# Kernel tuning notes

Hardware: AMD Instinct MI355X
Metric: run time of the kernel (lower is better)

## Reference

```python
import jax, jax.numpy as jnp
import numpy as np

N_NODES = 100000
N_EDGES = 3200000
EMBED_DIM = 64
BATCH = 16384


def setup_inputs() -> dict:
    key = jax.random.key(0)
    k1, k2, k3, k4 = jax.random.split(key, 4)
    gcn_weight = jax.random.normal(k1, (N_NODES, EMBED_DIM), dtype=jnp.float32) * 0.1
    gcn_bias = jnp.zeros((EMBED_DIM,), dtype=jnp.float32)
    linear_weight = jax.random.normal(k2, (N_NODES, 1), dtype=jnp.float32) * 0.1
    linear_bias = jnp.zeros((1,), dtype=jnp.float32)
    edge_index = jax.random.randint(k3, (2, N_EDGES), 0, N_NODES, dtype=jnp.int64)
    interaction_pairs = jax.random.randint(k4, (BATCH, 2), 0, N_NODES, dtype=jnp.int64)
    return {
        "gcn_weight": gcn_weight,
        "gcn_bias": gcn_bias,
        "linear_weight": linear_weight,
        "linear_bias": linear_bias,
        "edge_index": edge_index,
        "interaction_pairs": interaction_pairs,
    }


def _gcn_conv_identity_features(gcn_weight, gcn_bias, edge_index):
    # Features X = I, so X @ W = W. GCNConv output = D^{-1/2}(A+I)D^{-1/2} W + b.
    src, dst = edge_index[0], edge_index[1]
    ones = jnp.ones((src.shape[0],), dtype=gcn_weight.dtype)
    # degree (with self loop) computed on destination nodes, as in PyG gcn_norm
    deg = jax.ops.segment_sum(ones, dst, num_segments=N_NODES) + 1.0
    dinv = jax.lax.rsqrt(deg)  # [N]
    norm = dinv[src] * dinv[dst]  # [E]
    msg = gcn_weight[src] * norm[:, None]  # [E, D] -- dominant memory traffic
    agg = jax.ops.segment_sum(msg, dst, num_segments=N_NODES)  # [N, D]
    # self-loop term: norm_ii = 1/deg[i]
    out = agg + gcn_weight * (dinv * dinv)[:, None] + gcn_bias
    return out


def reference(gcn_weight, gcn_bias, linear_weight, linear_bias, edge_index, interaction_pairs):
    node_emb = _gcn_conv_identity_features(gcn_weight, gcn_bias, edge_index)  # [N, D]
    e = node_emb[interaction_pairs]  # [B, 2, D] gather
    # FM pairwise interaction: 0.5 * sum_d ((sum_f e)^2 - sum_f e^2)
    sum_sq = jnp.square(jnp.sum(e, axis=1))  # [B, D]
    sq_sum = jnp.sum(jnp.square(e), axis=1)  # [B, D]
    fm = 0.5 * jnp.sum(sum_sq - sq_sum, axis=1, keepdims=True)  # [B, 1]
    # FeaturesLinear: sum of per-node scalar embeddings + bias
    lin = jnp.sum(linear_weight[interaction_pairs], axis=1) + linear_bias  # [B, 1]
    return jnp.squeeze(lin + fm, axis=1)  # [B]
```

## Files before the change

### kernel.cpp

```cpp
#include <hip/hip_runtime.h>

#define N_NODES 100000
#define N_EDGES 3200000
#define BATCH 16384
#define MAX_SLOTS 32768

#define NW 12500
#define NW4 3125
#define SLICES 256
#define EPS2 12500
#define I4PS2 3125

#define NBUCK 512
#define BCAP 4096
#define BCAP_SH 12
#define EBCAP 4608
#define EBCAP4 1152

#define HIST_THREADS 1024
#define HGSIZE (SLICES * HIST_THREADS)

#define OFF_SLOT      0
#define OFF_DINV      400000
#define OFF_NODELIST  800000
#define OFF_GCUR      931072
#define OFF_PARTIALS  933120
#define OFF_WH        13733120
#define OFF_BINS      26533120
#define OFF_EMB       34921728

__device__ __forceinline__ unsigned bfr(float f) {
    unsigned u = __float_as_uint(f);
    return (u + 0x7FFFu + ((u >> 16) & 1u)) >> 16;
}
__device__ __forceinline__ float bfx(unsigned h) {
    return __uint_as_float(h << 16);
}

__global__ void k_flags(const int* __restrict__ pairs, unsigned* __restrict__ slot,
                        int* __restrict__ nodelist, unsigned* __restrict__ gcur) {
    int i = blockIdx.x * blockDim.x + threadIdx.x;
    if (i < NBUCK) gcur[i] = (unsigned)(i << BCAP_SH);
    if (i < 2 * BATCH) {
        int n = pairs[i];
        nodelist[i] = n;
        slot[n] = (unsigned)(i + 1);
    }
}

__device__ __forceinline__ int cert(int d, const unsigned* __restrict__ slot,
                                    const int* __restrict__ nodelist) {
    unsigned r = slot[d];
    unsigned idx = r - 1u;
    if (idx < (unsigned)MAX_SLOTS && nodelist[idx] == d) return (int)idx;
    return -1;
}

__global__ void k_hist(const int* __restrict__ src, const int* __restrict__ dst,
                       const unsigned* __restrict__ slot, const int* __restrict__ nodelist,
                       unsigned* __restrict__ partials, unsigned* __restrict__ gcur,
                       unsigned* __restrict__ bins,
                       const float4* __restrict__ w4, uint4* __restrict__ wh4) {
    __shared__ unsigned h[NW];
    __shared__ unsigned ebuf[EBCAP];
    __shared__ int lc[NBUCK];
    __shared__ int base[NBUCK];
    __shared__ int ecnt;
    int g = blockIdx.x;
    int tid = threadIdx.x;
    int lane = tid & 63;
    uint4* h4 = (uint4*)h;
    for (int i = tid; i < NW4; i += HIST_THREADS) h4[i] = make_uint4(0u, 0u, 0u, 0u);
    if (tid < NBUCK) lc[tid] = 0;
    if (tid == 0) ecnt = 0;
    __syncthreads();
    const int4* d4 = (const int4*)(dst + g * EPS2);
    const int4* s4 = (const int4*)(src + g * EPS2);
    for (int i = tid; i < I4PS2; i += HIST_THREADS) {
        int4 v = d4[i];
        int4 s = s4[i];
        atomicAdd(&h[v.x >> 3], 1u << ((v.x & 7) << 2));
        atomicAdd(&h[v.y >> 3], 1u << ((v.y & 7) << 2));
        atomicAdd(&h[v.z >> 3], 1u << ((v.z & 7) << 2));
        atomicAdd(&h[v.w >> 3], 1u << ((v.w & 7) << 2));
#define STAGE(dc, sc)                                                          \
        {                                                                      \
            int t = cert(dc, slot, nodelist);                                  \
            unsigned long long mk = __ballot(t >= 0);                          \
            int bs = 0;                                                        \
            if (lane == 0) bs = atomicAdd(&ecnt, (int)__popcll(mk));           \
            bs = __shfl(bs, 0, 64);                                            \
            if (t >= 0) {                                                      \
                int off = bs + (int)__popcll(mk & ((1ull << lane) - 1ull));    \
                if (off < EBCAP) {                                             \
                    ebuf[off] = ((unsigned)t << 17) | (unsigned)(sc);          \
                    atomicAdd(&lc[t >> 6], 1);                                 \
                }                                                              \
            }                                                                  \
        }
        STAGE(v.x, s.x)
        STAGE(v.y, s.y)
        STAGE(v.z, s.z)
        STAGE(v.w, s.w)
#undef STAGE
    }
    __syncthreads();
    uint4* outp4 = (uint4*)(partials + (unsigned)g * NW);
    for (int i = tid; i < NW4; i += HIST_THREADS) outp4[i] = h4[i];
    if (tid < NBUCK) {
        base[tid] = (int)atomicAdd(&gcur[tid], (unsigned)lc[tid]);
        lc[tid] = 0;
    }
    __syncthreads();
    int ne = ecnt;
    if (ne > EBCAP) ne = EBCAP;
    const uint4* ebuf4 = (const uint4*)ebuf;
    for (int j4 = tid; j4 * 4 < ne; j4 += HIST_THREADS) {
        uint4 e4 = ebuf4[j4];
#define FLUSH(ee, kk)                                                          \
        if (j4 * 4 + kk < ne) {                                                \
            unsigned e = (ee);                                                 \
            int b = (int)(e >> 23);                               \
            int r = atomicAdd(&lc[b], 1);                                      \
            unsigned pos = (unsigned)base[b] + (unsigned)r;                    \
            if (pos < (unsigned)((b + 1) << BCAP_SH)) bins[pos] = e;           \
        }
        FLUSH(e4.x, 0)
        FLUSH(e4.y, 1)
        FLUSH(e4.z, 2)
        FLUSH(e4.w, 3)
#undef FLUSH
    }
    for (int k = g * HIST_THREADS + tid; k < N_NODES * 8; k += HGSIZE) {
        float4 va = w4[k * 2];
        float4 vb = w4[k * 2 + 1];
        uint4 o;
        o.x = bfr(va.x) | (bfr(va.y) << 16);
        o.y = bfr(va.z) | (bfr(va.w) << 16);
        o.z = bfr(vb.x) | (bfr(vb.y) << 16);
        o.w = bfr(vb.z) | (bfr(vb.w) << 16);
        wh4[k] = o;
    }
}

__global__ void k_mid(const unsigned* __restrict__ partials, float* __restrict__ dinv) {
    __shared__ unsigned pA[256], pB[256], pC[256], pD[256];
    int blk = blockIdx.x;
    int wi = threadIdx.x & 31, sg = threadIdx.x >> 5;
    int w = blk * 32 + wi;
    unsigned A = 0, B = 0, C = 0, D = 0;
    if (w < NW) {
        const unsigned* q = partials + w;
#pragma unroll
        for (int ch = 0; ch < 2; ++ch) {
            unsigned x = 0, y = 0;
#pragma unroll
            for (int k = 0; k < 16; ++k) {
                unsigned v = q[(unsigned)(sg * 32 + ch * 16 + k) * NW];
                x += v & 0x0F0F0F0Fu;
                y += (v >> 4) & 0x0F0F0F0Fu;
            }
            A += x & 0x00FF00FFu;
            B += (x >> 8) & 0x00FF00FFu;
            C += y & 0x00FF00FFu;
            D += (y >> 8) & 0x00FF00FFu;
        }
    }
    pA[threadIdx.x] = A; pB[threadIdx.x] = B; pC[threadIdx.x] = C; pD[threadIdx.x] = D;
    __syncthreads();
    if (threadIdx.x < 32 && w < NW) {
        unsigned sA = 0, sB = 0, sC = 0, sD = 0;
#pragma unroll
        for (int k = 0; k < 8; ++k) {
            sA += pA[k * 32 + wi]; sB += pB[k * 32 + wi];
            sC += pC[k * 32 + wi]; sD += pD[k * 32 + wi];
        }
        float4 d0, d1;
        d0.x = rsqrtf((float)(sA & 0xFFFFu) + 1.0f);
        d0.y = rsqrtf((float)(sC & 0xFFFFu) + 1.0f);
        d0.z = rsqrtf((float)(sB & 0xFFFFu) + 1.0f);
        d0.w = rsqrtf((float)(sD & 0xFFFFu) + 1.0f);
        d1.x = rsqrtf((float)(sA >> 16) + 1.0f);
        d1.y = rsqrtf((float)(sC >> 16) + 1.0f);
        d1.z = rsqrtf((float)(sB >> 16) + 1.0f);
        d1.w = rsqrtf((float)(sD >> 16) + 1.0f);
        ((float4*)dinv)[w * 2] = d0;
        ((float4*)dinv)[w * 2 + 1] = d1;
    }
}

__global__ void k_gfuse(const unsigned* __restrict__ gcur, const unsigned* __restrict__ bins,
                        const int* __restrict__ nodelist, const uint4* __restrict__ wh4,
                        const float* __restrict__ dinv, const float4* __restrict__ bias4,
                        uint4* __restrict__ emb4) {
    __shared__ unsigned ebuf2[BCAP];
    __shared__ int lc[64], st[64];
    int b = blockIdx.x;
    int tid = threadIdx.x;
    int cnt = (int)(gcur[b] - (unsigned)(b << BCAP_SH));
    if (cnt > BCAP) cnt = BCAP;
    const unsigned* bp = bins + ((unsigned)b << BCAP_SH);
    if (tid < 64) lc[tid] = 0;
    __syncthreads();
    for (int j = tid; j < cnt; j += 1024) atomicAdd(&lc[(bp[j] >> 17) & 63], 1);
    __syncthreads();
    if (tid < 64) st[tid] = lc[tid];
    __syncthreads();
    for (int off = 1; off < 64; off <<= 1) {
        int v = (tid < 64 && tid >= off) ? st[tid - off] : 0;
        __syncthreads();
        if (tid < 64) st[tid] += v;
        __syncthreads();
    }
    if (tid < 64) {
        st[tid] -= lc[tid];
        lc[tid] = st[tid];
    }
    __syncthreads();
    for (int j = tid; j < cnt; j += 1024) {
        unsigned e = bp[j];
        int r = atomicAdd(&lc[(e >> 17) & 63], 1);
        ebuf2[r] = e & 0x1FFFFu;
    }
    __syncthreads();
    int wave = tid >> 6, lane = tid & 63;
    int rg = lane >> 3, dp = lane & 7;
#pragma unroll 1
    for (int q = 0; q < 4; ++q) {
        int sl = wave * 4 + q;
        int s0 = st[sl];
        int cn = lc[sl] - s0;
        double a0 = 0., a1 = 0., a2 = 0., a3 = 0., a4 = 0., a5 = 0., a6 = 0., a7 = 0.;
        int j = 0;
        for (; j + 16 <= cn; j += 16) {
            int e0 = (int)ebuf2[s0 + j + rg];
            int e1 = (int)ebuf2[s0 + j + 8 + rg];
            float dv0 = dinv[e0], dv1 = dinv[e1];
            uint4 oa = wh4[(e0 << 3) + dp];
            uint4 ob = wh4[(e1 << 3) + dp];
            a0 += (double)(bfx(oa.x) * dv0 + bfx(ob.x) * dv1);
            a1 += (double)(bfx(oa.x >> 16) * dv0 + bfx(ob.x >> 16) * dv1);
            a2 += (double)(bfx(oa.y) * dv0 + bfx(ob.y) * dv1);
            a3 += (double)(bfx(oa.y >> 16) * dv0 + bfx(ob.y >> 16) * dv1);
            a4 += (double)(bfx(oa.z) * dv0 + bfx(ob.z) * dv1);
            a5 += (double)(bfx(oa.z >> 16) * dv0 + bfx(ob.z >> 16) * dv1);
            a6 += (double)(bfx(oa.w) * dv0 + bfx(ob.w) * dv1);
            a7 += (double)(bfx(oa.w >> 16) * dv0 + bfx(ob.w >> 16) * dv1);
        }
        for (; j < cn; j += 8) {
            if (rg < cn - j) {
                int e0 = (int)ebuf2[s0 + j + rg];
                float dv0 = dinv[e0];
                uint4 oa = wh4[(e0 << 3) + dp];
                a0 += (double)(bfx(oa.x) * dv0);
                a1 += (double)(bfx(oa.x >> 16) * dv0);
                a2 += (double)(bfx(oa.y) * dv0);
                a3 += (double)(bfx(oa.y >> 16) * dv0);
                a4 += (double)(bfx(oa.z) * dv0);
                a5 += (double)(bfx(oa.z >> 16) * dv0);
                a6 += (double)(bfx(oa.w) * dv0);
                a7 += (double)(bfx(oa.w >> 16) * dv0);
            }
        }
#pragma unroll
        for (int m = 8; m <= 32; m <<= 1) {
            a0 += __shfl_xor(a0, m, 64); a1 += __shfl_xor(a1, m, 64);
            a2 += __shfl_xor(a2, m, 64); a3 += __shfl_xor(a3, m, 64);
            a4 += __shfl_xor(a4, m, 64); a5 += __shfl_xor(a5, m, 64);
            a6 += __shfl_xor(a6, m, 64); a7 += __shfl_xor(a7, m, 64);
        }
        if (rg == 0) {
            int gslot = (b << 6) + sl;
            int n = nodelist[gslot];
            float dn = dinv[n];
            uint4 u = wh4[(n << 3) + dp];
            float4 b0 = bias4[dp * 2], b1 = bias4[dp * 2 + 1];
            float r0 = ((float)a0 + bfx(u.x) * dn) * dn + b0.x;
            float r1 = ((float)a1 + bfx(u.x >> 16) * dn) * dn + b0.y;
            float r2 = ((float)a2 + bfx(u.y) * dn) * dn + b0.z;
            float r3 = ((float)a3 + bfx(u.y >> 16) * dn) * dn + b0.w;
            float r4 = ((float)a4 + bfx(u.z) * dn) * dn + b1.x;
            float r5 = ((float)a5 + bfx(u.z >> 16) * dn) * dn + b1.y;
            float r6 = ((float)a6 + bfx(u.w) * dn) * dn + b1.z;
            float r7 = ((float)a7 + bfx(u.w >> 16) * dn) * dn + b1.w;
            uint4 o;
            o.x = bfr(r0) | (bfr(r1) << 16);
            o.y = bfr(r2) | (bfr(r3) << 16);
            o.z = bfr(r4) | (bfr(r5) << 16);
            o.w = bfr(r6) | (bfr(r7) << 16);
            emb4[(gslot << 3) + dp] = o;
        }
    }
}

__global__ void k_final(const int* __restrict__ pairs, const unsigned* __restrict__ slot,
                        const uint2* __restrict__ emb2, const float* __restrict__ lw,
                        const float* __restrict__ lb, float* __restrict__ out) {
    int p = (blockIdx.x * blockDim.x + threadIdx.x) >> 4;
    int li = threadIdx.x & 15;
    if (p >= BATCH) return;
    int a = pairs[p * 2], b = pairs[p * 2 + 1];
    int sa = (int)slot[a] - 1;
    int sb = (int)slot[b] - 1;
    uint2 ua = emb2[(sa << 4) + li];
    uint2 ub = emb2[(sb << 4) + li];
    float prod = bfx(ua.x) * bfx(ub.x) + bfx(ua.x >> 16) * bfx(ub.x >> 16)
               + bfx(ua.y) * bfx(ub.y) + bfx(ua.y >> 16) * bfx(ub.y >> 16);
#pragma unroll
    for (int m = 1; m <= 8; m <<= 1) prod += __shfl_xor(prod, m, 64);
    if (li == 0) out[p] = lw[a] + lw[b] + lb[0] + prod;
}

extern "C" void kernel_launch(void* const* d_in, const int* in_sizes, int n_in,
                              void* d_out, int out_size, void* d_ws, size_t ws_size,
                              hipStream_t stream) {
    const float* gcn_weight    = (const float*)d_in[0];
    const float* gcn_bias      = (const float*)d_in[1];
    const float* linear_weight = (const float*)d_in[2];
    const float* linear_bias   = (const float*)d_in[3];
    const int*   edge_index    = (const int*)d_in[4];
    const int*   pairs         = (const int*)d_in[5];
    float* out = (float*)d_out;

    char* ws = (char*)d_ws;
    unsigned* slot      = (unsigned*)(ws + OFF_SLOT);
    float*    dinv      = (float*)   (ws + OFF_DINV);
    int*      nodelist  = (int*)     (ws + OFF_NODELIST);
    unsigned* gcur      = (unsigned*)(ws + OFF_GCUR);
    unsigned* partials  = (unsigned*)(ws + OFF_PARTIALS);
    uint4*    wh4       = (uint4*)   (ws + OFF_WH);
    unsigned* bins      = (unsigned*)(ws + OFF_BINS);
    uint4*    emb4      = (uint4*)   (ws + OFF_EMB);
    uint2*    emb2      = (uint2*)   (ws + OFF_EMB);

    const int* src_arr = edge_index;
    const int* dst_arr = edge_index + N_EDGES;

    k_flags<<<64, 512, 0, stream>>>(pairs, slot, nodelist, gcur);
    k_hist<<<SLICES, HIST_THREADS, 0, stream>>>(src_arr, dst_arr, slot, nodelist,
                                                partials, gcur, bins,
                                                (const float4*)gcn_weight, wh4);
    k_mid<<<391, 256, 0, stream>>>(partials, dinv);
    k_gfuse<<<NBUCK, 1024, 0, stream>>>(gcur, bins, nodelist, wh4,
                                        dinv, (const float4*)gcn_bias, emb4);
    k_final<<<1024, 256, 0, stream>>>(pairs, slot, emb2, linear_weight, linear_bias, out);
}
```

Measured before the change: 161.5 us.

## Double histogram slices and zero slot table to drop nodelist verification

Raises the number of histogram blocks from 256 to 512, each handling about half as many edges, and resizes the partials buffer, workspace offsets and the k_mid reduction loop to match. Adds a kernel that zeroes the slot table every call, so k_hist can test slot[d] != 0 directly instead of also checking nodelist. That removes one dependent global load per edge. In exchange it adds a kernel launch, doubles the partial-histogram traffic that k_mid has to reduce, and shrinks the per-block edge buffer, which raises the risk of dropping entries if a block overflows it.

```diff
diff --git a/kernel.cpp b/kernel.cpp
--- a/kernel.cpp
+++ b/kernel.cpp
@@ -7,15 +7,14 @@
 
 #define NW 12500
 #define NW4 3125
-#define SLICES 256
-#define EPS2 12500
-#define I4PS2 3125
+#define SLICES 512
+#define NI4 800000
+#define M4 1563
 
 #define NBUCK 512
 #define BCAP 4096
 #define BCAP_SH 12
-#define EBCAP 4608
-#define EBCAP4 1152
+#define EBCAP 2560
 
 #define HIST_THREADS 1024
 #define HGSIZE (SLICES * HIST_THREADS)
@@ -25,9 +24,9 @@
 #define OFF_NODELIST  800000
 #define OFF_GCUR      931072
 #define OFF_PARTIALS  933120
-#define OFF_WH        13733120
-#define OFF_BINS      26533120
-#define OFF_EMB       34921728
+#define OFF_WH        26533120
+#define OFF_BINS      39333120
+#define OFF_EMB       47721728
 
 __device__ __forceinline__ unsigned bfr(float f) {
     unsigned u = __float_as_uint(f);
@@ -35,6 +34,11 @@
 }
 __device__ __forceinline__ float bfx(unsigned h) {
     return __uint_as_float(h << 16);
+}
+
+__global__ void k_zero(unsigned* __restrict__ slot) {
+    int i = blockIdx.x * blockDim.x + threadIdx.x;
+    if (i < N_NODES) slot[i] = 0u;
 }
 
 __global__ void k_flags(const int* __restrict__ pairs, unsigned* __restrict__ slot,
@@ -48,16 +52,8 @@
     }
 }
 
-__device__ __forceinline__ int cert(int d, const unsigned* __restrict__ slot,
-                                    const int* __restrict__ nodelist) {
-    unsigned r = slot[d];
-    unsigned idx = r - 1u;
-    if (idx < (unsigned)MAX_SLOTS && nodelist[idx] == d) return (int)idx;
-    return -1;
-}
-
 __global__ void k_hist(const int* __restrict__ src, const int* __restrict__ dst,
-                       const unsigned* __restrict__ slot, const int* __restrict__ nodelist,
+                       const unsigned* __restrict__ slot,
                        unsigned* __restrict__ partials, unsigned* __restrict__ gcur,
                        unsigned* __restrict__ bins,
                        const float4* __restrict__ w4, uint4* __restrict__ wh4) {
@@ -74,9 +70,12 @@
     if (tid < NBUCK) lc[tid] = 0;
     if (tid == 0) ecnt = 0;
     __syncthreads();
-    const int4* d4 = (const int4*)(dst + g * EPS2);
-    const int4* s4 = (const int4*)(src + g * EPS2);
-    for (int i = tid; i < I4PS2; i += HIST_THREADS) {
+    const int4* d4 = (const int4*)dst;
+    const int4* s4 = (const int4*)src;
+    int start4 = g * M4;
+    int end4 = start4 + M4;
+    if (end4 > NI4) end4 = NI4;
+    for (int i = start4 + tid; i < end4; i += HIST_THREADS) {
         int4 v = d4[i];
         int4 s = s4[i];
         atomicAdd(&h[v.x >> 3], 1u << ((v.x & 7) << 2));
@@ -85,12 +84,13 @@
         atomicAdd(&h[v.w >> 3], 1u << ((v.w & 7) << 2));
 #define STAGE(dc, sc)                                                          \
         {                                                                      \
-            int t = cert(dc, slot, nodelist);                                  \
-            unsigned long long mk = __ballot(t >= 0);                          \
+            unsigned r = slot[dc];                                             \
+            unsigned long long mk = __ballot(r != 0u);                         \
             int bs = 0;                                                        \
             if (lane == 0) bs = atomicAdd(&ecnt, (int)__popcll(mk));           \
             bs = __shfl(bs, 0, 64);                                            \
-            if (t >= 0) {                                                      \
+            if (r != 0u) {                                                     \
+                int t = (int)r - 1;                                            \
                 int off = bs + (int)__popcll(mk & ((1ull << lane) - 1ull));    \
                 if (off < EBCAP) {                                             \
                     ebuf[off] = ((unsigned)t << 17) | (unsigned)(sc);          \
@@ -152,11 +152,11 @@
     if (w < NW) {
         const unsigned* q = partials + w;
 #pragma unroll
-        for (int ch = 0; ch < 2; ++ch) {
+        for (int ch = 0; ch < 4; ++ch) {
             unsigned x = 0, y = 0;
 #pragma unroll
             for (int k = 0; k < 16; ++k) {
-                unsigned v = q[(unsigned)(sg * 32 + ch * 16 + k) * NW];
+                unsigned v = q[(unsigned)(sg * 64 + ch * 16 + k) * NW];
                 x += v & 0x0F0F0F0Fu;
                 y += (v >> 4) & 0x0F0F0F0Fu;
             }
@@ -336,8 +336,9 @@
     const int* src_arr = edge_index;
     const int* dst_arr = edge_index + N_EDGES;
 
+    k_zero<<<128, 1024, 0, stream>>>(slot);
     k_flags<<<64, 512, 0, stream>>>(pairs, slot, nodelist, gcur);
-    k_hist<<<SLICES, HIST_THREADS, 0, stream>>>(src_arr, dst_arr, slot, nodelist,
+    k_hist<<<SLICES, HIST_THREADS, 0, stream>>>(src_arr, dst_arr, slot,
                                                 partials, gcur, bins,
                                                 (const float4*)gcn_weight, wh4);
     k_mid<<<391, 256, 0, stream>>>(partials, dinv);
```

After: 164.9 us. 2.1% more time.

## Coarsen edge buckets to 128 slots and batch ballot offset reservation

Applied to the files above, without the earlier changes.

The number of destination buckets is halved and each bucket now holds 128 target slots, so the histogram kernel does fewer global cursor atomics and its flush writes land in larger, more contiguous regions. The gather kernel launches two blocks per bucket, each handling one half of the slots, and both blocks redundantly re-sort the whole bucket in shared memory. The hist kernel also computes all four ballots first and reserves space in the staging buffer with one shared atomic per iteration instead of four. The cost is duplicated sorting work in the gather kernel and larger shared buffers per block.

```diff
diff --git a/kernel.cpp b/kernel.cpp
--- a/kernel.cpp
+++ b/kernel.cpp
@@ -11,11 +11,10 @@
 #define EPS2 12500
 #define I4PS2 3125
 
-#define NBUCK 512
-#define BCAP 4096
-#define BCAP_SH 12
+#define NBUCK 256
+#define BCAP 8192
+#define BCAP_SH 13
 #define EBCAP 4608
-#define EBCAP4 1152
 
 #define HIST_THREADS 1024
 #define HGSIZE (SLICES * HIST_THREADS)
@@ -76,6 +75,8 @@
     __syncthreads();
     const int4* d4 = (const int4*)(dst + g * EPS2);
     const int4* s4 = (const int4*)(src + g * EPS2);
+    unsigned long long lm = (1ull << lane) - 1ull;
+#pragma unroll 2
     for (int i = tid; i < I4PS2; i += HIST_THREADS) {
         int4 v = d4[i];
         int4 s = s4[i];
@@ -83,26 +84,37 @@
         atomicAdd(&h[v.y >> 3], 1u << ((v.y & 7) << 2));
         atomicAdd(&h[v.z >> 3], 1u << ((v.z & 7) << 2));
         atomicAdd(&h[v.w >> 3], 1u << ((v.w & 7) << 2));
-#define STAGE(dc, sc)                                                          \
-        {                                                                      \
-            int t = cert(dc, slot, nodelist);                                  \
-            unsigned long long mk = __ballot(t >= 0);                          \
-            int bs = 0;                                                        \
-            if (lane == 0) bs = atomicAdd(&ecnt, (int)__popcll(mk));           \
-            bs = __shfl(bs, 0, 64);                                            \
-            if (t >= 0) {                                                      \
-                int off = bs + (int)__popcll(mk & ((1ull << lane) - 1ull));    \
-                if (off < EBCAP) {                                             \
-                    ebuf[off] = ((unsigned)t << 17) | (unsigned)(sc);          \
-                    atomicAdd(&lc[t >> 6], 1);                                 \
-                }                                                              \
-            }                                                                  \
-        }
-        STAGE(v.x, s.x)
-        STAGE(v.y, s.y)
-        STAGE(v.z, s.z)
-        STAGE(v.w, s.w)
-#undef STAGE
+        int t0 = cert(v.x, slot, nodelist);
+        int t1 = cert(v.y, slot, nodelist);
+        int t2 = cert(v.z, slot, nodelist);
+        int t3 = cert(v.w, slot, nodelist);
+        unsigned long long m0 = __ballot(t0 >= 0);
+        unsigned long long m1 = __ballot(t1 >= 0);
+        unsigned long long m2 = __ballot(t2 >= 0);
+        unsigned long long m3 = __ballot(t3 >= 0);
+        int c0 = (int)__popcll(m0);
+        int c1 = (int)__popcll(m1);
+        int c2 = (int)__popcll(m2);
+        int c3 = (int)__popcll(m3);
+        int bs = 0;
+        if (lane == 0) bs = atomicAdd(&ecnt, c0 + c1 + c2 + c3);
+        bs = __shfl(bs, 0, 64);
+        if (t0 >= 0) {
+            int off = bs + (int)__popcll(m0 & lm);
+            if (off < EBCAP) { ebuf[off] = ((unsigned)t0 << 17) | (unsigned)s.x; atomicAdd(&lc[t0 >> 7], 1); }
+        }
+        if (t1 >= 0) {
+            int off = bs + c0 + (int)__popcll(m1 & lm);
+            if (off < EBCAP) { ebuf[off] = ((unsigned)t1 << 17) | (unsigned)s.y; atomicAdd(&lc[t1 >> 7], 1); }
+        }
+        if (t2 >= 0) {
+            int off = bs + c0 + c1 + (int)__popcll(m2 & lm);
+            if (off < EBCAP) { ebuf[off] = ((unsigned)t2 << 17) | (unsigned)s.z; atomicAdd(&lc[t2 >> 7], 1); }
+        }
+        if (t3 >= 0) {
+            int off = bs + c0 + c1 + c2 + (int)__popcll(m3 & lm);
+            if (off < EBCAP) { ebuf[off] = ((unsigned)t3 << 17) | (unsigned)s.w; atomicAdd(&lc[t3 >> 7], 1); }
+        }
     }
     __syncthreads();
     uint4* outp4 = (uint4*)(partials + (unsigned)g * NW);
@@ -120,7 +132,7 @@
 #define FLUSH(ee, kk)                                                          \
         if (j4 * 4 + kk < ne) {                                                \
             unsigned e = (ee);                                                 \
-            int b = (int)(e >> 23);                               \
+            int b = (int)(e >> 24);                               \
             int r = atomicAdd(&lc[b], 1);                                      \
             unsigned pos = (unsigned)base[b] + (unsigned)r;                    \
             if (pos < (unsigned)((b + 1) << BCAP_SH)) bins[pos] = e;           \
@@ -194,32 +206,33 @@
                         const float* __restrict__ dinv, const float4* __restrict__ bias4,
                         uint4* __restrict__ emb4) {
     __shared__ unsigned ebuf2[BCAP];
-    __shared__ int lc[64], st[64];
-    int b = blockIdx.x;
+    __shared__ int lc[128], st[128];
+    int b = blockIdx.x >> 1;
+    int half = blockIdx.x & 1;
     int tid = threadIdx.x;
     int cnt = (int)(gcur[b] - (unsigned)(b << BCAP_SH));
     if (cnt > BCAP) cnt = BCAP;
     const unsigned* bp = bins + ((unsigned)b << BCAP_SH);
-    if (tid < 64) lc[tid] = 0;
-    __syncthreads();
-    for (int j = tid; j < cnt; j += 1024) atomicAdd(&lc[(bp[j] >> 17) & 63], 1);
-    __syncthreads();
-    if (tid < 64) st[tid] = lc[tid];
-    __syncthreads();
-    for (int off = 1; off < 64; off <<= 1) {
-        int v = (tid < 64 && tid >= off) ? st[tid - off] : 0;
+    if (tid < 128) lc[tid] = 0;
+    __syncthreads();
+    for (int j = tid; j < cnt; j += 1024) atomicAdd(&lc[(bp[j] >> 17) & 127], 1);
+    __syncthreads();
+    if (tid < 128) st[tid] = lc[tid];
+    __syncthreads();
+    for (int off = 1; off < 128; off <<= 1) {
+        int v = (tid < 128 && tid >= off) ? st[tid - off] : 0;
         __syncthreads();
-        if (tid < 64) st[tid] += v;
+        if (tid < 128) st[tid] += v;
         __syncthreads();
     }
-    if (tid < 64) {
+    if (tid < 128) {
         st[tid] -= lc[tid];
         lc[tid] = st[tid];
     }
     __syncthreads();
     for (int j = tid; j < cnt; j += 1024) {
         unsigned e = bp[j];
-        int r = atomicAdd(&lc[(e >> 17) & 63], 1);
+        int r = atomicAdd(&lc[(e >> 17) & 127], 1);
         ebuf2[r] = e & 0x1FFFFu;
     }
     __syncthreads();
@@ -227,7 +240,7 @@
     int rg = lane >> 3, dp = lane & 7;
 #pragma unroll 1
     for (int q = 0; q < 4; ++q) {
-        int sl = wave * 4 + q;
+        int sl = half * 64 + wave * 4 + q;
         int s0 = st[sl];
         int cn = lc[sl] - s0;
         double a0 = 0., a1 = 0., a2 = 0., a3 = 0., a4 = 0., a5 = 0., a6 = 0., a7 = 0.;
@@ -270,7 +283,7 @@
             a6 += __shfl_xor(a6, m, 64); a7 += __shfl_xor(a7, m, 64);
         }
         if (rg == 0) {
-            int gslot = (b << 6) + sl;
+            int gslot = (b << 7) + sl;
             int n = nodelist[gslot];
             float dn = dinv[n];
             uint4 u = wh4[(n << 3) + dp];
@@ -341,7 +354,7 @@
                                                 partials, gcur, bins,
                                                 (const float4*)gcn_weight, wh4);
     k_mid<<<391, 256, 0, stream>>>(partials, dinv);
-    k_gfuse<<<NBUCK, 1024, 0, stream>>>(gcur, bins, nodelist, wh4,
-                                        dinv, (const float4*)gcn_bias, emb4);
+    k_gfuse<<<NBUCK * 2, 1024, 0, stream>>>(gcur, bins, nodelist, wh4,
+                                            dinv, (const float4*)gcn_bias, emb4);
     k_final<<<1024, 256, 0, stream>>>(pairs, slot, emb2, linear_weight, linear_bias, out);
 }
```

Measured after the change: 159.6 us. Within noise of the previous version (-1.2%).
